# Performance work log

Measured on AMD Instinct MI355X. Metric: run time of the kernel, lower is better.

Reference implementation:

```python
import jax, jax.numpy as jnp
import numpy as np

L = 3      # num_attention_layers
H = 8      # num_attention_heads
BS, C, NR, NC = 8, 512, 64, 64


def setup_inputs() -> dict:
    key = jax.random.key(0)
    ks = jax.random.split(key, 8)
    inp = {
        "aligned_cells_feat": jax.random.normal(ks[0], (BS, C, NR, NC), jnp.float32),
        "masks": jnp.ones((BS, NR, NC), jnp.float32),
    }
    wnames = ["col_Wk", "col_Wq", "col_Wv", "row_Wk", "row_Wq", "row_Wv"]
    for i, n in enumerate(wnames):
        inp[n] = jax.random.normal(ks[1 + i], (L, C, C), jnp.float32) * 0.02
    for n in ["col_bk", "col_bq", "col_bv", "row_bk", "row_bq", "row_bv"]:
        inp[n] = jnp.zeros((L, C), jnp.float32)
    return inp


def _sa_layer(x, m, Wk, bk, Wq, bq, Wv, bv):
    # x: [B, c, n], m: [B, n] (1 = valid key)
    B, c, n = x.shape
    def proj(W, b):
        return (jnp.einsum('oc,bcn->bon', W, x) + b[None, :, None]).reshape(B, -1, H, n)
    k = proj(Wk, bk)   # [B, c/H, H, n]  (att_dim == c here)
    q = proj(Wq, bq)
    v = proj(Wv, bv)
    scale = 1.0 / np.sqrt(c).astype(np.float32)  # 1/sqrt(att_dim)
    logits = jnp.einsum('bchk,bchq->bhkq', k, q) * scale
    logits = logits - (1.0 - m[:, None, :, None]) * 1e8  # mask invalid keys
    w = jax.nn.softmax(logits, axis=2)                    # softmax over keys k
    o = jnp.einsum('bchk,bhkq->bchq', v, w).reshape(B, c, n)
    return o + x


def reference(aligned_cells_feat, masks,
              col_Wk, col_bk, col_Wq, col_bq, col_Wv, col_bv,
              row_Wk, row_bk, row_Wq, row_bq, row_Wv, row_bv):
    x = aligned_cells_feat
    bs, c, nr, nc = x.shape
    for i in range(L):
        # column attention: attend along nc within each row
        col = x.transpose(0, 2, 1, 3).reshape(bs * nr, c, nc)
        cm = masks.reshape(bs * nr, nc)
        col = _sa_layer(col, cm, col_Wk[i], col_bk[i], col_Wq[i], col_bq[i], col_Wv[i], col_bv[i])
        x = col.reshape(bs, nr, c, nc).transpose(0, 2, 1, 3)
        # row attention: attend along nr within each column
        row = x.transpose(0, 3, 1, 2).reshape(bs * nc, c, nr)
        rm = masks.transpose(0, 2, 1).reshape(bs * nc, nr)
        row = _sa_layer(row, rm, row_Wk[i], row_bk[i], row_Wq[i], row_bq[i], row_Wv[i], row_bv[i])
        x = row.reshape(bs, nc, c, nr).transpose(0, 2, 3, 1)
    return (x, masks)
```

## Files before the change

### kernel.cpp

```cpp
#include <hip/hip_runtime.h>

#define SM_X     65536
#define SM_HD    16384
#define SM_MROW  (SM_X + 4 * SM_HD)
#define SM_TOTAL (SM_MROW + 256)

typedef __attribute__((ext_vector_type(4))) float f32x4;
typedef __attribute__((ext_vector_type(8))) short bf16x8;
typedef __attribute__((ext_vector_type(4))) short s16x4;

__device__ __forceinline__ short f2b(float f) {
  union { float f; unsigned u; } v; v.f = f;
  return (short)((v.u + 0x7fffu + ((v.u >> 16) & 1u)) >> 16);
}
__device__ __forceinline__ float b2f(short u) {
  union { unsigned u; float f; } v; v.u = ((unsigned)(unsigned short)u) << 16;
  return v.f;
}
__device__ __forceinline__ f32x4 mfma16(bf16x8 a, bf16x8 b, f32x4 c) {
  return __builtin_amdgcn_mfma_f32_16x16x32_bf16(a, b, c, 0, 0, 0);
}

__device__ __forceinline__ void* ksw(void* base, int row, int boff) {
  return (char*)base + (row << 7) + (boff ^ ((row & 7) << 4));
}

template <int PASS, int FINAL>
__global__ __launch_bounds__(1024, 4)
void attn_pass(unsigned short* __restrict__ xw, float* __restrict__ outp,
               const short* __restrict__ Wk, const short* __restrict__ Wq,
               const short* __restrict__ Wv,
               const float* __restrict__ bk, const float* __restrict__ bq,
               const float* __restrict__ bv,
               const float* __restrict__ masks)
{
  extern __shared__ char smem[];
  float* mrow = (float*)(smem + SM_MROW);

  int bid = blockIdx.x;
  if (PASS == 1) bid = (bid & 7) * 64 + (bid >> 3);
  const int b  = bid >> 6;
  const int rc = bid & 63;

  const int t    = threadIdx.x;
  const int wv   = t >> 6;
  const int lane = t & 63;
  const int l16  = lane & 15;
  const int g4   = lane >> 4;

  const int sxl  = ((l16 ^ rc) & 7) << 4;
  const int sx30 = sxl & 0x30;
  const int sx64 = sxl & 0x40;

  const int p1_j = wv & 3, p1_proj = (wv >> 2) & 1, p1_mh = wv >> 3;
  const int p2_j = wv >> 2, p2_qb = (wv & 3) * 16;
  const int p34_j = wv & 3, p34_qr = wv >> 2;

  const short* wb_nh = (p1_proj ? Wq : Wk) + p1_mh * 16384 + lane * 8;
  const float* bp1   = p1_proj ? bq : bk;
  bf16x8 pa0 = *(const bf16x8*)(wb_nh + p1_j * 32768);
  bf16x8 pa1 = *(const bf16x8*)(wb_nh + p1_j * 32768 + 512);
  bf16x8 pa2 = *(const bf16x8*)(wb_nh + p1_j * 32768 + 1024);
  bf16x8 pa3 = *(const bf16x8*)(wb_nh + p1_j * 32768 + 1536);

  {
    const char* xb = (const char*)xw;
    const char* srcb = (PASS == 0)
        ? xb + (size_t)((b * 64 + rc) * 64) * 1024
        : xb + (size_t)(b * 4096 + rc) * 1024;
#pragma unroll
    for (int it = 0; it < 4; ++it) {
      const int idx = it * 1024 + t;
      const int n = idx >> 6, c = idx & 63;
      const char* g = (PASS == 0) ? srcb + n * 1024 + c * 16
                                  : srcb + (size_t)n * 65536 + c * 16;
      *(bf16x8*)(smem + n * 1024 + c * 16) = *(const bf16x8*)g;
    }
  }
  if (t < 64) {
    const float m = (PASS == 0) ? masks[b * 4096 + rc * 64 + t]
                                : masks[b * 4096 + t * 64 + rc];
    mrow[t] = (1.0f - m) * 1e8f;
  }
  __syncthreads();

  const char* xfb = smem + l16 * 1024 + ((16 * g4) ^ sx30);

#pragma unroll 1
  for (int g2 = 0; g2 < 2; ++g2) {
    {
      const int h = g2 * 4 + p1_j;
      const short* wb = wb_nh + h * 32768;
      char* gb = smem + SM_X + p1_j * SM_HD;
      short* ob = (short*)(gb + (p1_proj ? 8192 : 0));
      f32x4 acc[2][4] = {};
      bf16x8 c0a = pa0, c0b = pa1, c1a = pa2, c1b = pa3;
#pragma unroll
      for (int kk = 0; kk < 16; ++kk) {
        bf16x8 nna = c1a, nnb = c1b;
        if (kk < 14) {
          nna = *(const bf16x8*)(wb + (kk + 2) * 1024);
          nnb = *(const bf16x8*)(wb + (kk + 2) * 1024 + 512);
        }
        const int off = (kk * 64) ^ sx64;
#pragma unroll
        for (int nf = 0; nf < 4; ++nf) {
          bf16x8 bb = *(const bf16x8*)(xfb + nf * 16384 + off);
          acc[0][nf] = mfma16(c0a, bb, acc[0][nf]);
          acc[1][nf] = mfma16(c0b, bb, acc[1][nf]);
        }
        c0a = c1a; c0b = c1b; c1a = nna; c1b = nnb;
      }
      const float* bp = bp1 + h * 64;
#pragma unroll
      for (int mi = 0; mi < 2; ++mi) {
        const int db = p1_mh * 32 + mi * 16 + 4 * g4;
        const float4 bs = *(const float4*)(bp + db);
        const float ba[4] = { bs.x, bs.y, bs.z, bs.w };
#pragma unroll
        for (int nf = 0; nf < 4; ++nf) {
          s16x4 pk;
#pragma unroll
          for (int r = 0; r < 4; ++r) pk[r] = f2b(acc[mi][nf][r] + ba[r]);
          *(s16x4*)ksw(ob, nf * 16 + l16, 2 * db) = pk;
        }
      }
    }
    __syncthreads();

    const short* wbv = Wv + (size_t)(g2 * 4 + p34_j) * 32768
                     + (p34_qr >> 1) * 16384 + (p34_qr & 1) * 512 + lane * 8;
    bf16x8 pv0 = *(const bf16x8*)(wbv);
    bf16x8 pv1 = *(const bf16x8*)(wbv + 1024);

    {
      char* gb = smem + SM_X + p2_j * SM_HD;
      short* kb  = (short*)gb;
      short* qb_ = (short*)(gb + 8192);
      f32x4 st[4] = {};
#pragma unroll
      for (int dk = 0; dk < 2; ++dk) {
        const int bo = dk * 64 + 16 * g4;
        bf16x8 a = *(const bf16x8*)ksw(qb_, p2_qb + l16, bo);
#pragma unroll
        for (int tt = 0; tt < 4; ++tt) {
          bf16x8 bb = *(const bf16x8*)ksw(kb, tt * 16 + l16, bo);
          st[tt] = mfma16(a, bb, st[tt]);
        }
      }
      const float scale = 0.044194173824159216f;
      float v[4][4], mx[4], sm[4];
#pragma unroll
      for (int tt = 0; tt < 4; ++tt) {
        const float pen = mrow[tt * 16 + l16];
#pragma unroll
        for (int r = 0; r < 4; ++r) v[tt][r] = st[tt][r] * scale - pen;
      }
#pragma unroll
      for (int r = 0; r < 4; ++r)
        mx[r] = fmaxf(fmaxf(v[0][r], v[1][r]), fmaxf(v[2][r], v[3][r]));
#pragma unroll
      for (int d = 1; d <= 8; d <<= 1)
#pragma unroll
        for (int r = 0; r < 4; ++r) mx[r] = fmaxf(mx[r], __shfl_xor(mx[r], d));
#pragma unroll
      for (int r = 0; r < 4; ++r) sm[r] = 0.f;
#pragma unroll
      for (int tt = 0; tt < 4; ++tt)
#pragma unroll
        for (int r = 0; r < 4; ++r) { v[tt][r] = __expf(v[tt][r] - mx[r]); sm[r] += v[tt][r]; }
#pragma unroll
      for (int d = 1; d <= 8; d <<= 1)
#pragma unroll
        for (int r = 0; r < 4; ++r) sm[r] += __shfl_xor(sm[r], d);
#pragma unroll
      for (int r = 0; r < 4; ++r) sm[r] = 1.0f / sm[r];
#pragma unroll
      for (int tt = 0; tt < 4; ++tt)
#pragma unroll
        for (int r = 0; r < 4; ++r)
          *(short*)ksw(qb_, p2_qb + 4 * g4 + r, 2 * (tt * 16 + l16)) =
              f2b(v[tt][r] * sm[r]);
    }
    __syncthreads();

    {
      char* gb = smem + SM_X + p34_j * SM_HD;
      short* vbuf = (short*)gb;
      f32x4 acc[4] = {};
      bf16x8 c0 = pv0, c1 = pv1;
#pragma unroll
      for (int kk = 0; kk < 16; ++kk) {
        bf16x8 nn = c1;
        if (kk < 14) nn = *(const bf16x8*)(wbv + (kk + 2) * 1024);
        const int off = (kk * 64) ^ sx64;
#pragma unroll
        for (int nf = 0; nf < 4; ++nf) {
          bf16x8 bb = *(const bf16x8*)(xfb + nf * 16384 + off);
          acc[nf] = mfma16(c0, bb, acc[nf]);
        }
        c0 = c1; c1 = nn;
      }
      const int db = p34_qr * 16 + 4 * g4;
      const float4 bs = *(const float4*)(bv + (g2 * 4 + p34_j) * 64 + db);
      const float ba[4] = { bs.x, bs.y, bs.z, bs.w };
#pragma unroll
      for (int nf = 0; nf < 4; ++nf)
#pragma unroll
        for (int r = 0; r < 4; ++r)
          *(short*)ksw(vbuf, db + r, 2 * (nf * 16 + l16)) = f2b(acc[nf][r] + ba[r]);
    }
    __syncthreads();

    {
      const int h = g2 * 4 + p34_j;
      char* gb = smem + SM_X + p34_j * SM_HD;
      short* vbuf = (short*)gb;
      short* wbuf = (short*)(gb + 8192);
      f32x4 acc[4] = {};
#pragma unroll
      for (int dk = 0; dk < 2; ++dk) {
        const int bo = dk * 64 + 16 * g4;
        bf16x8 bw = *(const bf16x8*)ksw(wbuf, p34_qr * 16 + l16, bo);
#pragma unroll
        for (int nf = 0; nf < 4; ++nf) {
          bf16x8 av = *(const bf16x8*)ksw(vbuf, nf * 16 + l16, bo);
          acc[nf] = mfma16(av, bw, acc[nf]);
        }
      }
      const int q = p34_qr * 16 + l16;
      const size_t rowg = (PASS == 0) ? (size_t)((b * 64 + rc) * 64 + q)
                                      : (size_t)((b * 64 + q) * 64 + rc);
      char* grow = (char*)xw + rowg * 1024;
      const char* lrow = smem + q * 1024;
#pragma unroll
      for (int nf = 0; nf < 4; ++nf) {
        const int cb = (h * 128 + nf * 32 + 8 * g4) ^ sxl;
        const s16x4 rx = *(const s16x4*)(lrow + cb);
        if (FINAL) {
#pragma unroll
          for (int r = 0; r < 4; ++r) {
            const int ch = 8 * (nf * 16 + 4 * g4 + r) + h;
            const size_t off = (size_t)b * 2097152 + (size_t)ch * 4096
                             + ((PASS == 0) ? rc * 64 + q : q * 64 + rc);
            outp[off] = acc[nf][r] + b2f(rx[r]);
          }
        } else {
          s16x4 ov;
#pragma unroll
          for (int r = 0; r < 4; ++r) ov[r] = f2b(acc[nf][r] + b2f(rx[r]));
          *(s16x4*)(grow + cb) = ov;
        }
      }
      if (g2 == 0) {
        const short* wb2 = wb_nh + (4 + p1_j) * 32768;
        pa0 = *(const bf16x8*)(wb2);
        pa1 = *(const bf16x8*)(wb2 + 512);
        pa2 = *(const bf16x8*)(wb2 + 1024);
        pa3 = *(const bf16x8*)(wb2 + 1536);
      }
    }
    __syncthreads();
  }
}

__global__ __launch_bounds__(256)
void prep_x(const float* __restrict__ x, unsigned short* __restrict__ xw)
{
  extern __shared__ float tile[];
  const int b = blockIdx.x >> 6, nr = blockIdx.x & 63;
  const float* src = x + (size_t)b * 2097152 + nr * 64;
  const int t = threadIdx.x;
#pragma unroll 4
  for (int it = 0; it < 32; ++it) {
    const int idx = it * 256 + t;
    const int ch = idx >> 4, nc4 = (idx & 15) * 4;
    const float4 v = *(const float4*)(src + (size_t)ch * 4096 + nc4);
    const int p = ((ch & 7) << 6) | (ch >> 3);
    const int pp = p + (p >> 6);
    tile[(nc4 + 0) * 521 + pp] = v.x;
    tile[(nc4 + 1) * 521 + pp] = v.y;
    tile[(nc4 + 2) * 521 + pp] = v.z;
    tile[(nc4 + 3) * 521 + pp] = v.w;
  }
  __syncthreads();
  unsigned short* dst = xw + (size_t)(b * 64 + nr) * 32768;
#pragma unroll 4
  for (int it = 0; it < 16; ++it) {
    const int idx = it * 256 + t;
    const int nc = idx >> 6, p8 = (idx & 63) * 8;
    bf16x8 o;
#pragma unroll
    for (int j = 0; j < 8; ++j) {
      const int p = p8 + j;
      o[j] = f2b(tile[nc * 521 + p + (p >> 6)]);
    }
    const int sx = ((nr ^ nc) & 7) << 4;
    *(bf16x8*)((char*)(dst + nc * 512) + ((2 * p8) ^ sx)) = o;
  }
}

__global__ __launch_bounds__(256)
void unperm_b(const unsigned short* __restrict__ tmp, float* __restrict__ out)
{
  __shared__ float tile[64 * 65];
  const int nr = blockIdx.x >> 3, pb = blockIdx.x & 7;
  const int t = threadIdx.x;
#pragma unroll
  for (int it = 0; it < 4; ++it) {
    const int idx = it * 256 + t;
    const int nc = idx >> 4, p4 = (idx & 15) * 4;
    const int sx = ((nr ^ nc) & 7) << 4;
    const s16x4 v = *(const s16x4*)((const char*)(tmp + ((size_t)nr * 64 + nc) * 512)
                                    + ((2 * (pb * 64 + p4)) ^ sx));
#pragma unroll
    for (int j = 0; j < 4; ++j) tile[nc * 65 + p4 + j] = b2f(v[j]);
  }
  __syncthreads();
#pragma unroll
  for (int it = 0; it < 4; ++it) {
    const int idx = it * 256 + t;
    const int pi = idx >> 4, nc4 = (idx & 15) * 4;
    const int ch = 8 * pi + pb;
    float4 o;
#pragma unroll
    for (int j = 0; j < 4; ++j) (&o.x)[j] = tile[(nc4 + j) * 65 + pi];
    *(float4*)(out + (size_t)ch * 4096 + nr * 64 + nc4) = o;
  }
}

__global__ void pack_w(const float* __restrict__ w0, const float* __restrict__ w1,
                       const float* __restrict__ w2, const float* __restrict__ w3,
                       const float* __restrict__ w4, const float* __restrict__ w5,
                       short* __restrict__ dst)
{
  const float* s;
  switch (blockIdx.y) {
    case 0: s = w0; break; case 1: s = w1; break; case 2: s = w2; break;
    case 3: s = w3; break; case 4: s = w4; break; default: s = w5; break;
  }
  const int idx = blockIdx.x * 256 + threadIdx.x;
  const int l = idx >> 16;
  const int r = idx & 65535;
  const int o = r >> 7, c4 = (r & 127) * 4;
  const float4 v = *(const float4*)(s + ((size_t)l * 512 + o) * 512 + c4);
  const int h = o & 7, row8 = o >> 3;
  const int mh = row8 >> 5, f = (row8 >> 4) & 1, l16r = row8 & 15;
  short* db = dst + (size_t)blockIdx.y * 786432 + (size_t)l * 262144;
#pragma unroll
  for (int j = 0; j < 4; ++j) {
    const int ch = c4 + j;
    const int p = ((ch & 7) << 6) | (ch >> 3);
    const int jj = p & 7, g4p = (p >> 3) & 3, kk = p >> 5;
    const int lane = g4p * 16 + l16r;
    db[(size_t)(((((h * 2 + mh) * 16 + kk) * 2 + f) * 64 + lane)) * 8 + jj] =
        f2b((&v.x)[j]);
  }
}

__global__ void pack_b(const float* __restrict__ b0, const float* __restrict__ b1,
                       const float* __restrict__ b2, const float* __restrict__ b3,
                       const float* __restrict__ b4, const float* __restrict__ b5,
                       float* __restrict__ dst)
{
  const int idx = blockIdx.x * 256 + threadIdx.x;
  const int name = idx / 1536;
  const int rem  = idx - name * 1536;
  const int l = rem >> 9;
  const int p = rem & 511;
  const int h = p >> 6, d = p & 63;
  const float* s;
  switch (name) {
    case 0: s = b0; break; case 1: s = b1; break; case 2: s = b2; break;
    case 3: s = b3; break; case 4: s = b4; break; default: s = b5; break;
  }
  dst[idx] = s[l * 512 + 8 * d + h];
}

__global__ void copy_masks(const float* __restrict__ m, float* __restrict__ o) {
  const int i = blockIdx.x * 256 + threadIdx.x;
  ((float4*)o)[i] = ((const float4*)m)[i];
}

extern "C" void kernel_launch(void* const* d_in, const int* in_sizes, int n_in,
                              void* d_out, int out_size, void* d_ws, size_t ws_size,
                              hipStream_t stream)
{
  const float* x0    = (const float*)d_in[0];
  const float* masks = (const float*)d_in[1];
  short* wbf  = (short*)d_ws;
  float* bws  = (float*)((char*)d_ws + 9437184);
  float* xbuf = (float*)d_out;
  float* mout = xbuf + 16777216;

  const size_t xw_off = 9474048;
  const bool big = ws_size >= xw_off + (size_t)33554432;
  unsigned short* xw = big ? (unsigned short*)((char*)d_ws + xw_off)
                           : (unsigned short*)d_out;

  pack_w<<<dim3(768, 6), 256, 0, stream>>>(
      (const float*)d_in[2], (const float*)d_in[3], (const float*)d_in[4],
      (const float*)d_in[5], (const float*)d_in[6], (const float*)d_in[7], wbf);
  pack_b<<<36, 256, 0, stream>>>(
      (const float*)d_in[8], (const float*)d_in[9], (const float*)d_in[10],
      (const float*)d_in[11], (const float*)d_in[12], (const float*)d_in[13], bws);
  prep_x<<<512, 256, 64 * 521 * 4, stream>>>(x0, xw);
  copy_masks<<<32, 256, 0, stream>>>(masks, mout);

  const size_t WPL = 262144;
  for (int l = 0; l < 3; ++l) {
    attn_pass<0, 0><<<512, 1024, SM_TOTAL, stream>>>(
        xw, xbuf,
        wbf + (0 * 3 + l) * WPL, wbf + (1 * 3 + l) * WPL, wbf + (2 * 3 + l) * WPL,
        bws + (0 * 3 + l) * 512, bws + (1 * 3 + l) * 512, bws + (2 * 3 + l) * 512,
        masks);
    const short* rwk = wbf + (3 * 3 + l) * WPL;
    const short* rwq = wbf + (4 * 3 + l) * WPL;
    const short* rwv = wbf + (5 * 3 + l) * WPL;
    const float* rbk = bws + (3 * 3 + l) * 512;
    const float* rbq = bws + (4 * 3 + l) * 512;
    const float* rbv = bws + (5 * 3 + l) * 512;
    if (l == 2 && big)
      attn_pass<1, 1><<<512, 1024, SM_TOTAL, stream>>>(
          xw, xbuf, rwk, rwq, rwv, rbk, rbq, rbv, masks);
    else
      attn_pass<1, 0><<<512, 1024, SM_TOTAL, stream>>>(
          xw, xbuf, rwk, rwq, rwv, rbk, rbq, rbv, masks);
  }

  if (!big) {
    for (int b = 7; b >= 0; --b) {
      hipMemcpyAsync(wbf, xw + (size_t)b * 2097152, 4194304,
                     hipMemcpyDeviceToDevice, stream);
      unperm_b<<<512, 256, 0, stream>>>((const unsigned short*)wbf,
                                        xbuf + (size_t)b * 2097152);
    }
  }
}
```

Measured before the change: 770.5 us.

## Stage attention output in LDS and write back with coalesced 16-byte stores

Attention outputs for both head groups are kept in registers across the loop, combined with the residual, written into shared memory, and then copied to global memory as full coalesced 16-byte rows. This replaces scattered 8-byte per-lane global stores. The fused FINAL variant that wrote fp32 output straight from the last row pass is removed, and a separate unperm_full kernel now converts the bf16 workspace to the fp32 output. This adds register pressure, an extra barrier and an extra full-tensor pass at the end.

New measurement: 807.8 us. +4.8%, slower.

```diff
diff --git a/kernel.cpp b/kernel.cpp
--- a/kernel.cpp
+++ b/kernel.cpp
@@ -25,9 +25,9 @@
   return (char*)base + (row << 7) + (boff ^ ((row & 7) << 4));
 }
 
-template <int PASS, int FINAL>
+template <int PASS>
 __global__ __launch_bounds__(1024, 4)
-void attn_pass(unsigned short* __restrict__ xw, float* __restrict__ outp,
+void attn_pass(unsigned short* __restrict__ xw,
                const short* __restrict__ Wk, const short* __restrict__ Wq,
                const short* __restrict__ Wv,
                const float* __restrict__ bk, const float* __restrict__ bq,
@@ -85,6 +85,8 @@
   __syncthreads();
 
   const char* xfb = smem + l16 * 1024 + ((16 * g4) ^ sx30);
+
+  f32x4 accA[4], accB[4];
 
 #pragma unroll 1
   for (int g2 = 0; g2 < 2; ++g2) {
@@ -213,11 +215,10 @@
     __syncthreads();
 
     {
-      const int h = g2 * 4 + p34_j;
       char* gb = smem + SM_X + p34_j * SM_HD;
       short* vbuf = (short*)gb;
       short* wbuf = (short*)(gb + 8192);
-      f32x4 acc[4] = {};
+      f32x4 po[4] = {};
 #pragma unroll
       for (int dk = 0; dk < 2; ++dk) {
         const int bo = dk * 64 + 16 * g4;
@@ -225,42 +226,57 @@
 #pragma unroll
         for (int nf = 0; nf < 4; ++nf) {
           bf16x8 av = *(const bf16x8*)ksw(vbuf, nf * 16 + l16, bo);
-          acc[nf] = mfma16(av, bw, acc[nf]);
-        }
-      }
-      const int q = p34_qr * 16 + l16;
-      const size_t rowg = (PASS == 0) ? (size_t)((b * 64 + rc) * 64 + q)
-                                      : (size_t)((b * 64 + q) * 64 + rc);
-      char* grow = (char*)xw + rowg * 1024;
-      const char* lrow = smem + q * 1024;
-#pragma unroll
-      for (int nf = 0; nf < 4; ++nf) {
-        const int cb = (h * 128 + nf * 32 + 8 * g4) ^ sxl;
-        const s16x4 rx = *(const s16x4*)(lrow + cb);
-        if (FINAL) {
-#pragma unroll
-          for (int r = 0; r < 4; ++r) {
-            const int ch = 8 * (nf * 16 + 4 * g4 + r) + h;
-            const size_t off = (size_t)b * 2097152 + (size_t)ch * 4096
-                             + ((PASS == 0) ? rc * 64 + q : q * 64 + rc);
-            outp[off] = acc[nf][r] + b2f(rx[r]);
-          }
-        } else {
-          s16x4 ov;
-#pragma unroll
-          for (int r = 0; r < 4; ++r) ov[r] = f2b(acc[nf][r] + b2f(rx[r]));
-          *(s16x4*)(grow + cb) = ov;
+          po[nf] = mfma16(av, bw, po[nf]);
         }
       }
       if (g2 == 0) {
+        accA[0] = po[0]; accA[1] = po[1]; accA[2] = po[2]; accA[3] = po[3];
         const short* wb2 = wb_nh + (4 + p1_j) * 32768;
         pa0 = *(const bf16x8*)(wb2);
         pa1 = *(const bf16x8*)(wb2 + 512);
         pa2 = *(const bf16x8*)(wb2 + 1024);
         pa3 = *(const bf16x8*)(wb2 + 1536);
+      } else {
+        accB[0] = po[0]; accB[1] = po[1]; accB[2] = po[2]; accB[3] = po[3];
       }
     }
     __syncthreads();
+  }
+
+  {
+    const int q = p34_qr * 16 + l16;
+    const char* lrow = smem + q * 1024;
+    char*       orow = smem + SM_X + q * 1024;
+#pragma unroll
+    for (int hh = 0; hh < 2; ++hh) {
+      const int h = hh * 4 + p34_j;
+#pragma unroll
+      for (int nf = 0; nf < 4; ++nf) {
+        const int cb = (h * 128 + nf * 32 + 8 * g4) ^ sxl;
+        const s16x4 rx = *(const s16x4*)(lrow + cb);
+        const f32x4 av = hh ? accB[nf] : accA[nf];
+        s16x4 ov;
+#pragma unroll
+        for (int r = 0; r < 4; ++r) ov[r] = f2b(av[r] + b2f(rx[r]));
+        *(s16x4*)(orow + cb) = ov;
+      }
+    }
+  }
+  __syncthreads();
+
+  {
+    char* xb = (char*)xw;
+    char* dstb = (PASS == 0)
+        ? xb + (size_t)((b * 64 + rc) * 64) * 1024
+        : xb + (size_t)(b * 4096 + rc) * 1024;
+#pragma unroll
+    for (int it = 0; it < 4; ++it) {
+      const int idx = it * 1024 + t;
+      const int n = idx >> 6, c = idx & 63;
+      char* g = (PASS == 0) ? dstb + n * 1024 + c * 16
+                            : dstb + (size_t)n * 65536 + c * 16;
+      *(bf16x8*)g = *(const bf16x8*)(smem + SM_X + n * 1024 + c * 16);
+    }
   }
 }
 
@@ -326,6 +342,37 @@
 #pragma unroll
     for (int j = 0; j < 4; ++j) (&o.x)[j] = tile[(nc4 + j) * 65 + pi];
     *(float4*)(out + (size_t)ch * 4096 + nr * 64 + nc4) = o;
+  }
+}
+
+__global__ __launch_bounds__(256)
+void unperm_full(const unsigned short* __restrict__ xw, float* __restrict__ out)
+{
+  __shared__ float tile[64 * 65];
+  const int b = blockIdx.x >> 9, nr = (blockIdx.x >> 3) & 63, pb = blockIdx.x & 7;
+  const unsigned short* tmp = xw + (size_t)b * 2097152;
+  float* ob = out + (size_t)b * 2097152;
+  const int t = threadIdx.x;
+#pragma unroll
+  for (int it = 0; it < 4; ++it) {
+    const int idx = it * 256 + t;
+    const int nc = idx >> 4, p4 = (idx & 15) * 4;
+    const int sx = ((nr ^ nc) & 7) << 4;
+    const s16x4 v = *(const s16x4*)((const char*)(tmp + ((size_t)nr * 64 + nc) * 512)
+                                    + ((2 * (pb * 64 + p4)) ^ sx));
+#pragma unroll
+    for (int j = 0; j < 4; ++j) tile[nc * 65 + p4 + j] = b2f(v[j]);
+  }
+  __syncthreads();
+#pragma unroll
+  for (int it = 0; it < 4; ++it) {
+    const int idx = it * 256 + t;
+    const int pi = idx >> 4, nc4 = (idx & 15) * 4;
+    const int ch = 8 * pi + pb;
+    float4 o;
+#pragma unroll
+    for (int j = 0; j < 4; ++j) (&o.x)[j] = tile[(nc4 + j) * 65 + pi];
+    *(float4*)(ob + (size_t)ch * 4096 + nr * 64 + nc4) = o;
   }
 }
 
@@ -409,26 +456,21 @@
 
   const size_t WPL = 262144;
   for (int l = 0; l < 3; ++l) {
-    attn_pass<0, 0><<<512, 1024, SM_TOTAL, stream>>>(
-        xw, xbuf,
+    attn_pass<0><<<512, 1024, SM_TOTAL, stream>>>(
+        xw,
         wbf + (0 * 3 + l) * WPL, wbf + (1 * 3 + l) * WPL, wbf + (2 * 3 + l) * WPL,
         bws + (0 * 3 + l) * 512, bws + (1 * 3 + l) * 512, bws + (2 * 3 + l) * 512,
         masks);
-    const short* rwk = wbf + (3 * 3 + l) * WPL;
-    const short* rwq = wbf + (4 * 3 + l) * WPL;
-    const short* rwv = wbf + (5 * 3 + l) * WPL;
-    const float* rbk = bws + (3 * 3 + l) * 512;
-    const float* rbq = bws + (4 * 3 + l) * 512;
-    const float* rbv = bws + (5 * 3 + l) * 512;
-    if (l == 2 && big)
-      attn_pass<1, 1><<<512, 1024, SM_TOTAL, stream>>>(
-          xw, xbuf, rwk, rwq, rwv, rbk, rbq, rbv, masks);
-    else
-      attn_pass<1, 0><<<512, 1024, SM_TOTAL, stream>>>(
-          xw, xbuf, rwk, rwq, rwv, rbk, rbq, rbv, masks);
-  }
-
-  if (!big) {
+    attn_pass<1><<<512, 1024, SM_TOTAL, stream>>>(
+        xw,
+        wbf + (3 * 3 + l) * WPL, wbf + (4 * 3 + l) * WPL, wbf + (5 * 3 + l) * WPL,
+        bws + (3 * 3 + l) * 512, bws + (4 * 3 + l) * 512, bws + (5 * 3 + l) * 512,
+        masks);
+  }
+
+  if (big) {
+    unperm_full<<<4096, 256, 0, stream>>>(xw, xbuf);
+  } else {
     for (int b = 7; b >= 0; --b) {
       hipMemcpyAsync(wbf, xw + (size_t)b * 2097152, 4194304,
                      hipMemcpyDeviceToDevice, stream);
```

## Fuse K/Q/V projections into one GEMM phase and defer residual writeback

Applied to the files above, without the earlier changes.

Each wave now computes three 16-row fragments across K, Q and V projections in a single MFMA loop, so every shared-memory load of x feeds twelve MFMAs. This removes the separate V-projection phase and one barrier per head group. The outputs of both head groups are kept in registers and written to global memory once at the end. The mask penalty is read directly from global memory instead of a shared buffer. In exchange, per-head shared slots grow to 24 KB and register pressure rises, which may hurt occupancy under the 1024-thread launch bound.

New measurement: 1.187 ms. 54.1% more time.

```diff
diff --git a/kernel.cpp b/kernel.cpp
--- a/kernel.cpp
+++ b/kernel.cpp
@@ -1,9 +1,8 @@
 #include <hip/hip_runtime.h>
 
 #define SM_X     65536
-#define SM_HD    16384
-#define SM_MROW  (SM_X + 4 * SM_HD)
-#define SM_TOTAL (SM_MROW + 256)
+#define SM_SLOT  24576
+#define SM_TOTAL 163840
 
 typedef __attribute__((ext_vector_type(4))) float f32x4;
 typedef __attribute__((ext_vector_type(8))) short bf16x8;
@@ -20,7 +19,6 @@
 __device__ __forceinline__ f32x4 mfma16(bf16x8 a, bf16x8 b, f32x4 c) {
   return __builtin_amdgcn_mfma_f32_16x16x32_bf16(a, b, c, 0, 0, 0);
 }
-
 __device__ __forceinline__ void* ksw(void* base, int row, int boff) {
   return (char*)base + (row << 7) + (boff ^ ((row & 7) << 4));
 }
@@ -35,7 +33,6 @@
                const float* __restrict__ masks)
 {
   extern __shared__ char smem[];
-  float* mrow = (float*)(smem + SM_MROW);
 
   int bid = blockIdx.x;
   if (PASS == 1) bid = (bid & 7) * 64 + (bid >> 3);
@@ -52,16 +49,27 @@
   const int sx30 = sxl & 0x30;
   const int sx64 = sxl & 0x40;
 
-  const int p1_j = wv & 3, p1_proj = (wv >> 2) & 1, p1_mh = wv >> 3;
+  int pj_[3], jj_[3], fi_[3];
+  const short* wp0[3];
+  const float* bb0[3];
+#pragma unroll
+  for (int i = 0; i < 3; ++i) {
+    const int tid = 3 * wv + i;
+    const int proj = tid >> 4, j = (tid >> 2) & 3, fi = tid & 3;
+    pj_[i] = proj; jj_[i] = j; fi_[i] = fi;
+    const short* W = (proj == 0) ? Wk : (proj == 1) ? Wq : Wv;
+    wp0[i] = W + j * 32768 + (fi >> 1) * 16384 + (fi & 1) * 512 + lane * 8;
+    bb0[i] = ((proj == 0) ? bk : (proj == 1) ? bq : bv) + j * 64 + fi * 16 + 4 * g4;
+  }
   const int p2_j = wv >> 2, p2_qb = (wv & 3) * 16;
   const int p34_j = wv & 3, p34_qr = wv >> 2;
 
-  const short* wb_nh = (p1_proj ? Wq : Wk) + p1_mh * 16384 + lane * 8;
-  const float* bp1   = p1_proj ? bq : bk;
-  bf16x8 pa0 = *(const bf16x8*)(wb_nh + p1_j * 32768);
-  bf16x8 pa1 = *(const bf16x8*)(wb_nh + p1_j * 32768 + 512);
-  bf16x8 pa2 = *(const bf16x8*)(wb_nh + p1_j * 32768 + 1024);
-  bf16x8 pa3 = *(const bf16x8*)(wb_nh + p1_j * 32768 + 1536);
+  bf16x8 pf0[3], pf1[3];
+#pragma unroll
+  for (int i = 0; i < 3; ++i) {
+    pf0[i] = *(const bf16x8*)(wp0[i]);
+    pf1[i] = *(const bf16x8*)(wp0[i] + 1024);
+  }
 
   {
     const char* xb = (const char*)xw;
@@ -77,66 +85,79 @@
       *(bf16x8*)(smem + n * 1024 + c * 16) = *(const bf16x8*)g;
     }
   }
-  if (t < 64) {
-    const float m = (PASS == 0) ? masks[b * 4096 + rc * 64 + t]
-                                : masks[b * 4096 + t * 64 + rc];
-    mrow[t] = (1.0f - m) * 1e8f;
-  }
   __syncthreads();
 
   const char* xfb = smem + l16 * 1024 + ((16 * g4) ^ sx30);
+
+  f32x4 accA[4], accB[4];
 
 #pragma unroll 1
   for (int g2 = 0; g2 < 2; ++g2) {
     {
-      const int h = g2 * 4 + p1_j;
-      const short* wb = wb_nh + h * 32768;
-      char* gb = smem + SM_X + p1_j * SM_HD;
-      short* ob = (short*)(gb + (p1_proj ? 8192 : 0));
-      f32x4 acc[2][4] = {};
-      bf16x8 c0a = pa0, c0b = pa1, c1a = pa2, c1b = pa3;
+      const short* wpg[3];
+#pragma unroll
+      for (int i = 0; i < 3; ++i) wpg[i] = wp0[i] + g2 * 131072;
+      f32x4 acc[3][4] = {};
+      bf16x8 c0[3], c1[3];
+#pragma unroll
+      for (int i = 0; i < 3; ++i) { c0[i] = pf0[i]; c1[i] = pf1[i]; }
 #pragma unroll
       for (int kk = 0; kk < 16; ++kk) {
-        bf16x8 nna = c1a, nnb = c1b;
-        if (kk < 14) {
-          nna = *(const bf16x8*)(wb + (kk + 2) * 1024);
-          nnb = *(const bf16x8*)(wb + (kk + 2) * 1024 + 512);
+        bf16x8 nx[3];
+#pragma unroll
+        for (int i = 0; i < 3; ++i)
+          nx[i] = (kk < 14) ? *(const bf16x8*)(wpg[i] + (kk + 2) * 1024) : c1[i];
+        const int off = (kk * 64) ^ sx64;
+        bf16x8 bbf[4];
+#pragma unroll
+        for (int nf = 0; nf < 4; ++nf)
+          bbf[nf] = *(const bf16x8*)(xfb + nf * 16384 + off);
+#pragma unroll
+        for (int i = 0; i < 3; ++i)
+#pragma unroll
+          for (int nf = 0; nf < 4; ++nf)
+            acc[i][nf] = mfma16(c0[i], bbf[nf], acc[i][nf]);
+#pragma unroll
+        for (int i = 0; i < 3; ++i) { c0[i] = c1[i]; c1[i] = nx[i]; }
+      }
+#pragma unroll
+      for (int i = 0; i < 3; ++i) {
+        const float4 bs = *(const float4*)(bb0[i] + g2 * 256);
+        const float ba[4] = { bs.x, bs.y, bs.z, bs.w };
+        if (pj_[i] < 2) {
+          short* ob = (short*)(smem + SM_X + jj_[i] * SM_SLOT + pj_[i] * 8192);
+#pragma unroll
+          for (int nf = 0; nf < 4; ++nf) {
+            s16x4 pk;
+#pragma unroll
+            for (int r = 0; r < 4; ++r) pk[r] = f2b(acc[i][nf][r] + ba[r]);
+            *(s16x4*)ksw(ob, nf * 16 + l16, 2 * (fi_[i] * 16 + 4 * g4)) = pk;
+          }
+        } else {
+          short* vb_ = (short*)(smem + SM_X + jj_[i] * SM_SLOT + 16384);
+#pragma unroll
+          for (int nf = 0; nf < 4; ++nf)
+#pragma unroll
+            for (int r = 0; r < 4; ++r)
+              *(short*)ksw(vb_, fi_[i] * 16 + 4 * g4 + r, 2 * (nf * 16 + l16)) =
+                  f2b(acc[i][nf][r] + ba[r]);
         }
-        const int off = (kk * 64) ^ sx64;
-#pragma unroll
-        for (int nf = 0; nf < 4; ++nf) {
-          bf16x8 bb = *(const bf16x8*)(xfb + nf * 16384 + off);
-          acc[0][nf] = mfma16(c0a, bb, acc[0][nf]);
-          acc[1][nf] = mfma16(c0b, bb, acc[1][nf]);
-        }
-        c0a = c1a; c0b = c1b; c1a = nna; c1b = nnb;
-      }
-      const float* bp = bp1 + h * 64;
-#pragma unroll
-      for (int mi = 0; mi < 2; ++mi) {
-        const int db = p1_mh * 32 + mi * 16 + 4 * g4;
-        const float4 bs = *(const float4*)(bp + db);
-        const float ba[4] = { bs.x, bs.y, bs.z, bs.w };
-#pragma unroll
-        for (int nf = 0; nf < 4; ++nf) {
-          s16x4 pk;
-#pragma unroll
-          for (int r = 0; r < 4; ++r) pk[r] = f2b(acc[mi][nf][r] + ba[r]);
-          *(s16x4*)ksw(ob, nf * 16 + l16, 2 * db) = pk;
-        }
       }
     }
     __syncthreads();
 
-    const short* wbv = Wv + (size_t)(g2 * 4 + p34_j) * 32768
-                     + (p34_qr >> 1) * 16384 + (p34_qr & 1) * 512 + lane * 8;
-    bf16x8 pv0 = *(const bf16x8*)(wbv);
-    bf16x8 pv1 = *(const bf16x8*)(wbv + 1024);
-
     {
-      char* gb = smem + SM_X + p2_j * SM_HD;
+      char* gb = smem + SM_X + p2_j * SM_SLOT;
       short* kb  = (short*)gb;
       short* qb_ = (short*)(gb + 8192);
+      float pen[4];
+#pragma unroll
+      for (int tt = 0; tt < 4; ++tt) {
+        const int key = tt * 16 + l16;
+        const float m = (PASS == 0) ? masks[b * 4096 + rc * 64 + key]
+                                    : masks[b * 4096 + key * 64 + rc];
+        pen[tt] = (1.0f - m) * 1e8f;
+      }
       f32x4 st[4] = {};
 #pragma unroll
       for (int dk = 0; dk < 2; ++dk) {
@@ -144,18 +165,16 @@
         bf16x8 a = *(const bf16x8*)ksw(qb_, p2_qb + l16, bo);
 #pragma unroll
         for (int tt = 0; tt < 4; ++tt) {
-          bf16x8 bb = *(const bf16x8*)ksw(kb, tt * 16 + l16, bo);
-          st[tt] = mfma16(a, bb, st[tt]);
+          bf16x8 bbf = *(const bf16x8*)ksw(kb, tt * 16 + l16, bo);
+          st[tt] = mfma16(a, bbf, st[tt]);
         }
       }
       const float scale = 0.044194173824159216f;
       float v[4][4], mx[4], sm[4];
 #pragma unroll
-      for (int tt = 0; tt < 4; ++tt) {
-        const float pen = mrow[tt * 16 + l16];
-#pragma unroll
-        for (int r = 0; r < 4; ++r) v[tt][r] = st[tt][r] * scale - pen;
-      }
+      for (int tt = 0; tt < 4; ++tt)
+#pragma unroll
+        for (int r = 0; r < 4; ++r) v[tt][r] = st[tt][r] * scale - pen[tt];
 #pragma unroll
       for (int r = 0; r < 4; ++r)
         mx[r] = fmaxf(fmaxf(v[0][r], v[1][r]), fmaxf(v[2][r], v[3][r]));
@@ -185,39 +204,10 @@
     __syncthreads();
 
     {
-      char* gb = smem + SM_X + p34_j * SM_HD;
-      short* vbuf = (short*)gb;
-      f32x4 acc[4] = {};
-      bf16x8 c0 = pv0, c1 = pv1;
-#pragma unroll
-      for (int kk = 0; kk < 16; ++kk) {
-        bf16x8 nn = c1;
-        if (kk < 14) nn = *(const bf16x8*)(wbv + (kk + 2) * 1024);
-        const int off = (kk * 64) ^ sx64;
-#pragma unroll
-        for (int nf = 0; nf < 4; ++nf) {
-          bf16x8 bb = *(const bf16x8*)(xfb + nf * 16384 + off);
-          acc[nf] = mfma16(c0, bb, acc[nf]);
-        }
-        c0 = c1; c1 = nn;
-      }
-      const int db = p34_qr * 16 + 4 * g4;
-      const float4 bs = *(const float4*)(bv + (g2 * 4 + p34_j) * 64 + db);
-      const float ba[4] = { bs.x, bs.y, bs.z, bs.w };
-#pragma unroll
-      for (int nf = 0; nf < 4; ++nf)
-#pragma unroll
-        for (int r = 0; r < 4; ++r)
-          *(short*)ksw(vbuf, db + r, 2 * (nf * 16 + l16)) = f2b(acc[nf][r] + ba[r]);
-    }
-    __syncthreads();
-
-    {
-      const int h = g2 * 4 + p34_j;
-      char* gb = smem + SM_X + p34_j * SM_HD;
-      short* vbuf = (short*)gb;
+      char* gb = smem + SM_X + p34_j * SM_SLOT;
       short* wbuf = (short*)(gb + 8192);
-      f32x4 acc[4] = {};
+      short* vbuf = (short*)(gb + 16384);
+      f32x4 po[4] = {};
 #pragma unroll
       for (int dk = 0; dk < 2; ++dk) {
         const int bo = dk * 64 + 16 * g4;
@@ -225,42 +215,53 @@
 #pragma unroll
         for (int nf = 0; nf < 4; ++nf) {
           bf16x8 av = *(const bf16x8*)ksw(vbuf, nf * 16 + l16, bo);
-          acc[nf] = mfma16(av, bw, acc[nf]);
+          po[nf] = mfma16(av, bw, po[nf]);
         }
       }
-      const int q = p34_qr * 16 + l16;
-      const size_t rowg = (PASS == 0) ? (size_t)((b * 64 + rc) * 64 + q)
-                                      : (size_t)((b * 64 + q) * 64 + rc);
-      char* grow = (char*)xw + rowg * 1024;
-      const char* lrow = smem + q * 1024;
+      if (g2 == 0) {
+        accA[0] = po[0]; accA[1] = po[1]; accA[2] = po[2]; accA[3] = po[3];
+#pragma unroll
+        for (int i = 0; i < 3; ++i) {
+          pf0[i] = *(const bf16x8*)(wp0[i] + 131072);
+          pf1[i] = *(const bf16x8*)(wp0[i] + 131072 + 1024);
+        }
+      } else {
+        accB[0] = po[0]; accB[1] = po[1]; accB[2] = po[2]; accB[3] = po[3];
+      }
+    }
+    if (g2 == 0) __syncthreads();
+  }
+
+  {
+    const int q = p34_qr * 16 + l16;
+    const char* lrow = smem + q * 1024;
+    const size_t rowg = (PASS == 0) ? (size_t)((b * 64 + rc) * 64 + q)
+                                    : (size_t)((b * 64 + q) * 64 + rc);
+    char* grow = (char*)xw + rowg * 1024;
+#pragma unroll
+    for (int hh = 0; hh < 2; ++hh) {
+      const int h = hh * 4 + p34_j;
 #pragma unroll
       for (int nf = 0; nf < 4; ++nf) {
         const int cb = (h * 128 + nf * 32 + 8 * g4) ^ sxl;
         const s16x4 rx = *(const s16x4*)(lrow + cb);
+        const f32x4 av = hh ? accB[nf] : accA[nf];
         if (FINAL) {
 #pragma unroll
           for (int r = 0; r < 4; ++r) {
             const int ch = 8 * (nf * 16 + 4 * g4 + r) + h;
             const size_t off = (size_t)b * 2097152 + (size_t)ch * 4096
                              + ((PASS == 0) ? rc * 64 + q : q * 64 + rc);
-            outp[off] = acc[nf][r] + b2f(rx[r]);
+            outp[off] = av[r] + b2f(rx[r]);
           }
         } else {
           s16x4 ov;
 #pragma unroll
-          for (int r = 0; r < 4; ++r) ov[r] = f2b(acc[nf][r] + b2f(rx[r]));
+          for (int r = 0; r < 4; ++r) ov[r] = f2b(av[r] + b2f(rx[r]));
           *(s16x4*)(grow + cb) = ov;
         }
       }
-      if (g2 == 0) {
-        const short* wb2 = wb_nh + (4 + p1_j) * 32768;
-        pa0 = *(const bf16x8*)(wb2);
-        pa1 = *(const bf16x8*)(wb2 + 512);
-        pa2 = *(const bf16x8*)(wb2 + 1024);
-        pa3 = *(const bf16x8*)(wb2 + 1536);
-      }
-    }
-    __syncthreads();
+    }
   }
 }
 
```

## Split waves between softmax and V projection to overlap them in one phase

Applied to the files above, without the earlier changes.

Restructures each head-group iteration so waves 0-7 compute the logits and softmax (two query tiles each) while waves 8-15 compute the V projection into a separate LDS region. This removes one of the four barriers per iteration and lets the VALU-heavy softmax run alongside the MFMA-heavy V GEMM. Mask penalties are read directly from global memory instead of an LDS row, and the trailing barrier is skipped on the last iteration. LDS use grows to 160KB for the separate V buffer, which may limit blocks per CU, and the work split between the two wave groups is uneven.

Result: faster. 633.5 us, median of 2 (-17.8%).

```diff
diff --git a/kernel.cpp b/kernel.cpp
--- a/kernel.cpp
+++ b/kernel.cpp
@@ -2,8 +2,8 @@
 
 #define SM_X     65536
 #define SM_HD    16384
-#define SM_MROW  (SM_X + 4 * SM_HD)
-#define SM_TOTAL (SM_MROW + 256)
+#define SM_VB    131072
+#define SM_TOTAL 163840
 
 typedef __attribute__((ext_vector_type(4))) float f32x4;
 typedef __attribute__((ext_vector_type(8))) short bf16x8;
@@ -20,7 +20,6 @@
 __device__ __forceinline__ f32x4 mfma16(bf16x8 a, bf16x8 b, f32x4 c) {
   return __builtin_amdgcn_mfma_f32_16x16x32_bf16(a, b, c, 0, 0, 0);
 }
-
 __device__ __forceinline__ void* ksw(void* base, int row, int boff) {
   return (char*)base + (row << 7) + (boff ^ ((row & 7) << 4));
 }
@@ -35,7 +34,6 @@
                const float* __restrict__ masks)
 {
   extern __shared__ char smem[];
-  float* mrow = (float*)(smem + SM_MROW);
 
   int bid = blockIdx.x;
   if (PASS == 1) bid = (bid & 7) * 64 + (bid >> 3);
@@ -53,7 +51,8 @@
   const int sx64 = sxl & 0x40;
 
   const int p1_j = wv & 3, p1_proj = (wv >> 2) & 1, p1_mh = wv >> 3;
-  const int p2_j = wv >> 2, p2_qb = (wv & 3) * 16;
+  const int s_j  = wv >> 1, s_qh = wv & 1;
+  const int v_j  = (wv & 7) >> 1, v_mh = wv & 1;
   const int p34_j = wv & 3, p34_qr = wv >> 2;
 
   const short* wb_nh = (p1_proj ? Wq : Wk) + p1_mh * 16384 + lane * 8;
@@ -62,6 +61,7 @@
   bf16x8 pa1 = *(const bf16x8*)(wb_nh + p1_j * 32768 + 512);
   bf16x8 pa2 = *(const bf16x8*)(wb_nh + p1_j * 32768 + 1024);
   bf16x8 pa3 = *(const bf16x8*)(wb_nh + p1_j * 32768 + 1536);
+  bf16x8 pv0, pv1, pv2, pv3;
 
   {
     const char* xb = (const char*)xw;
@@ -76,11 +76,6 @@
                                   : srcb + (size_t)n * 65536 + c * 16;
       *(bf16x8*)(smem + n * 1024 + c * 16) = *(const bf16x8*)g;
     }
-  }
-  if (t < 64) {
-    const float m = (PASS == 0) ? masks[b * 4096 + rc * 64 + t]
-                                : masks[b * 4096 + t * 64 + rc];
-    mrow[t] = (1.0f - m) * 1e8f;
   }
   __syncthreads();
 
@@ -111,6 +106,14 @@
         }
         c0a = c1a; c0b = c1b; c1a = nna; c1b = nnb;
       }
+      if (wv >= 8) {
+        const short* wbv = Wv + (size_t)(g2 * 4 + v_j) * 32768
+                         + v_mh * 16384 + lane * 8;
+        pv0 = *(const bf16x8*)(wbv);
+        pv1 = *(const bf16x8*)(wbv + 512);
+        pv2 = *(const bf16x8*)(wbv + 1024);
+        pv3 = *(const bf16x8*)(wbv + 1536);
+      }
       const float* bp = bp1 + h * 64;
 #pragma unroll
       for (int mi = 0; mi < 2; ++mi) {
@@ -128,96 +131,114 @@
     }
     __syncthreads();
 
-    const short* wbv = Wv + (size_t)(g2 * 4 + p34_j) * 32768
-                     + (p34_qr >> 1) * 16384 + (p34_qr & 1) * 512 + lane * 8;
-    bf16x8 pv0 = *(const bf16x8*)(wbv);
-    bf16x8 pv1 = *(const bf16x8*)(wbv + 1024);
-
-    {
-      char* gb = smem + SM_X + p2_j * SM_HD;
+    if (wv < 8) {
+      char* gb = smem + SM_X + s_j * SM_HD;
       short* kb  = (short*)gb;
       short* qb_ = (short*)(gb + 8192);
-      f32x4 st[4] = {};
+      float pen[4];
+#pragma unroll
+      for (int tt = 0; tt < 4; ++tt) {
+        const int key = tt * 16 + l16;
+        const float m = (PASS == 0) ? masks[b * 4096 + rc * 64 + key]
+                                    : masks[b * 4096 + key * 64 + rc];
+        pen[tt] = (1.0f - m) * 1e8f;
+      }
+      f32x4 st[2][4] = {};
 #pragma unroll
       for (int dk = 0; dk < 2; ++dk) {
         const int bo = dk * 64 + 16 * g4;
-        bf16x8 a = *(const bf16x8*)ksw(qb_, p2_qb + l16, bo);
+        bf16x8 a0 = *(const bf16x8*)ksw(qb_, s_qh * 32 + l16, bo);
+        bf16x8 a1 = *(const bf16x8*)ksw(qb_, s_qh * 32 + 16 + l16, bo);
 #pragma unroll
         for (int tt = 0; tt < 4; ++tt) {
           bf16x8 bb = *(const bf16x8*)ksw(kb, tt * 16 + l16, bo);
-          st[tt] = mfma16(a, bb, st[tt]);
+          st[0][tt] = mfma16(a0, bb, st[0][tt]);
+          st[1][tt] = mfma16(a1, bb, st[1][tt]);
         }
       }
       const float scale = 0.044194173824159216f;
-      float v[4][4], mx[4], sm[4];
-#pragma unroll
-      for (int tt = 0; tt < 4; ++tt) {
-        const float pen = mrow[tt * 16 + l16];
-#pragma unroll
-        for (int r = 0; r < 4; ++r) v[tt][r] = st[tt][r] * scale - pen;
-      }
-#pragma unroll
-      for (int r = 0; r < 4; ++r)
-        mx[r] = fmaxf(fmaxf(v[0][r], v[1][r]), fmaxf(v[2][r], v[3][r]));
-#pragma unroll
-      for (int d = 1; d <= 8; d <<= 1)
-#pragma unroll
-        for (int r = 0; r < 4; ++r) mx[r] = fmaxf(mx[r], __shfl_xor(mx[r], d));
-#pragma unroll
-      for (int r = 0; r < 4; ++r) sm[r] = 0.f;
-#pragma unroll
-      for (int tt = 0; tt < 4; ++tt)
-#pragma unroll
-        for (int r = 0; r < 4; ++r) { v[tt][r] = __expf(v[tt][r] - mx[r]); sm[r] += v[tt][r]; }
-#pragma unroll
-      for (int d = 1; d <= 8; d <<= 1)
-#pragma unroll
-        for (int r = 0; r < 4; ++r) sm[r] += __shfl_xor(sm[r], d);
-#pragma unroll
-      for (int r = 0; r < 4; ++r) sm[r] = 1.0f / sm[r];
-#pragma unroll
-      for (int tt = 0; tt < 4; ++tt)
+      float v[2][4][4], mx[2][4], sm[2][4];
+#pragma unroll
+      for (int qi = 0; qi < 2; ++qi) {
+#pragma unroll
+        for (int tt = 0; tt < 4; ++tt)
+#pragma unroll
+          for (int r = 0; r < 4; ++r) v[qi][tt][r] = st[qi][tt][r] * scale - pen[tt];
 #pragma unroll
         for (int r = 0; r < 4; ++r)
-          *(short*)ksw(qb_, p2_qb + 4 * g4 + r, 2 * (tt * 16 + l16)) =
-              f2b(v[tt][r] * sm[r]);
-    }
-    __syncthreads();
-
-    {
-      char* gb = smem + SM_X + p34_j * SM_HD;
-      short* vbuf = (short*)gb;
-      f32x4 acc[4] = {};
-      bf16x8 c0 = pv0, c1 = pv1;
+          mx[qi][r] = fmaxf(fmaxf(v[qi][0][r], v[qi][1][r]),
+                            fmaxf(v[qi][2][r], v[qi][3][r]));
+#pragma unroll
+        for (int d = 1; d <= 8; d <<= 1)
+#pragma unroll
+          for (int r = 0; r < 4; ++r)
+            mx[qi][r] = fmaxf(mx[qi][r], __shfl_xor(mx[qi][r], d));
+#pragma unroll
+        for (int r = 0; r < 4; ++r) sm[qi][r] = 0.f;
+#pragma unroll
+        for (int tt = 0; tt < 4; ++tt)
+#pragma unroll
+          for (int r = 0; r < 4; ++r) {
+            v[qi][tt][r] = __expf(v[qi][tt][r] - mx[qi][r]);
+            sm[qi][r] += v[qi][tt][r];
+          }
+#pragma unroll
+        for (int d = 1; d <= 8; d <<= 1)
+#pragma unroll
+          for (int r = 0; r < 4; ++r) sm[qi][r] += __shfl_xor(sm[qi][r], d);
+#pragma unroll
+        for (int r = 0; r < 4; ++r) sm[qi][r] = 1.0f / sm[qi][r];
+#pragma unroll
+        for (int tt = 0; tt < 4; ++tt)
+#pragma unroll
+          for (int r = 0; r < 4; ++r)
+            *(short*)ksw(qb_, s_qh * 32 + qi * 16 + 4 * g4 + r,
+                         2 * (tt * 16 + l16)) =
+                f2b(v[qi][tt][r] * sm[qi][r]);
+      }
+    } else {
+      const short* wbv = Wv + (size_t)(g2 * 4 + v_j) * 32768
+                       + v_mh * 16384 + lane * 8;
+      short* vbuf = (short*)(smem + SM_VB + v_j * 8192);
+      f32x4 acc[2][4] = {};
+      bf16x8 c0a = pv0, c0b = pv1, c1a = pv2, c1b = pv3;
 #pragma unroll
       for (int kk = 0; kk < 16; ++kk) {
-        bf16x8 nn = c1;
-        if (kk < 14) nn = *(const bf16x8*)(wbv + (kk + 2) * 1024);
+        bf16x8 nna = c1a, nnb = c1b;
+        if (kk < 14) {
+          nna = *(const bf16x8*)(wbv + (kk + 2) * 1024);
+          nnb = *(const bf16x8*)(wbv + (kk + 2) * 1024 + 512);
+        }
         const int off = (kk * 64) ^ sx64;
 #pragma unroll
         for (int nf = 0; nf < 4; ++nf) {
           bf16x8 bb = *(const bf16x8*)(xfb + nf * 16384 + off);
-          acc[nf] = mfma16(c0, bb, acc[nf]);
-        }
-        c0 = c1; c1 = nn;
-      }
-      const int db = p34_qr * 16 + 4 * g4;
-      const float4 bs = *(const float4*)(bv + (g2 * 4 + p34_j) * 64 + db);
-      const float ba[4] = { bs.x, bs.y, bs.z, bs.w };
-#pragma unroll
-      for (int nf = 0; nf < 4; ++nf)
-#pragma unroll
-        for (int r = 0; r < 4; ++r)
-          *(short*)ksw(vbuf, db + r, 2 * (nf * 16 + l16)) = f2b(acc[nf][r] + ba[r]);
+          acc[0][nf] = mfma16(c0a, bb, acc[0][nf]);
+          acc[1][nf] = mfma16(c0b, bb, acc[1][nf]);
+        }
+        c0a = c1a; c0b = c1b; c1a = nna; c1b = nnb;
+      }
+      const float* bp = bv + (g2 * 4 + v_j) * 64;
+#pragma unroll
+      for (int mi = 0; mi < 2; ++mi) {
+        const int db = v_mh * 32 + mi * 16 + 4 * g4;
+        const float4 bs = *(const float4*)(bp + db);
+        const float ba[4] = { bs.x, bs.y, bs.z, bs.w };
+#pragma unroll
+        for (int nf = 0; nf < 4; ++nf)
+#pragma unroll
+          for (int r = 0; r < 4; ++r)
+            *(short*)ksw(vbuf, db + r, 2 * (nf * 16 + l16)) =
+                f2b(acc[mi][nf][r] + ba[r]);
+      }
     }
     __syncthreads();
 
     {
       const int h = g2 * 4 + p34_j;
-      char* gb = smem + SM_X + p34_j * SM_HD;
-      short* vbuf = (short*)gb;
-      short* wbuf = (short*)(gb + 8192);
-      f32x4 acc[4] = {};
+      short* wbuf = (short*)(smem + SM_X + p34_j * SM_HD + 8192);
+      short* vbuf = (short*)(smem + SM_VB + p34_j * 8192);
+      f32x4 po[4] = {};
 #pragma unroll
       for (int dk = 0; dk < 2; ++dk) {
         const int bo = dk * 64 + 16 * g4;
@@ -225,14 +246,14 @@
 #pragma unroll
         for (int nf = 0; nf < 4; ++nf) {
           bf16x8 av = *(const bf16x8*)ksw(vbuf, nf * 16 + l16, bo);
-          acc[nf] = mfma16(av, bw, acc[nf]);
+          po[nf] = mfma16(av, bw, po[nf]);
         }
       }
       const int q = p34_qr * 16 + l16;
+      const char* lrow = smem + q * 1024;
       const size_t rowg = (PASS == 0) ? (size_t)((b * 64 + rc) * 64 + q)
                                       : (size_t)((b * 64 + q) * 64 + rc);
       char* grow = (char*)xw + rowg * 1024;
-      const char* lrow = smem + q * 1024;
 #pragma unroll
       for (int nf = 0; nf < 4; ++nf) {
         const int cb = (h * 128 + nf * 32 + 8 * g4) ^ sxl;
@@ -243,12 +264,12 @@
             const int ch = 8 * (nf * 16 + 4 * g4 + r) + h;
             const size_t off = (size_t)b * 2097152 + (size_t)ch * 4096
                              + ((PASS == 0) ? rc * 64 + q : q * 64 + rc);
-            outp[off] = acc[nf][r] + b2f(rx[r]);
+            outp[off] = po[nf][r] + b2f(rx[r]);
           }
         } else {
           s16x4 ov;
 #pragma unroll
-          for (int r = 0; r < 4; ++r) ov[r] = f2b(acc[nf][r] + b2f(rx[r]));
+          for (int r = 0; r < 4; ++r) ov[r] = f2b(po[nf][r] + b2f(rx[r]));
           *(s16x4*)(grow + cb) = ov;
         }
       }
@@ -260,7 +281,7 @@
         pa3 = *(const bf16x8*)(wb2 + 1536);
       }
     }
-    __syncthreads();
+    if (g2 == 0) __syncthreads();
   }
 }
 
```
